# Kernel optimization log

Hardware: AMD Instinct MI355X
Metric: run time of the kernel (lower is better)

Reference implementation:

```python
import jax, jax.numpy as jnp
import numpy as np

T = 4096      # total tokens (flattened batch)
H = 4096      # input_size / hidden dim
O = 4096      # output_size_per_partition
R = 16        # max_lora_rank
L = 8         # max_loras
S = 8         # num_lora_seqs


def setup_inputs() -> dict:
    key = jax.random.key(0)
    k_x, k_w, k_b, k_a, k_bb, k_idx = jax.random.split(key, 6)
    x = jax.random.normal(k_x, (T, H), dtype=jnp.float32)
    weight = jax.random.normal(k_w, (O, H), dtype=jnp.float32) * 0.02
    bias = jax.random.normal(k_b, (O,), dtype=jnp.float32)
    lora_a = jax.random.normal(k_a, (L, H, R), dtype=jnp.float32) * 0.02
    lora_b = jax.random.normal(k_bb, (L, R, O), dtype=jnp.float32) * 0.02
    # indices[i] = (start_idx[i], lora_idx[i]); indices[-1,0] = T (end sentinel).
    # Segment i covers tokens [start[i], start[i+1]) and uses adapter lora_idx[i].
    starts = jnp.arange(S + 1, dtype=jnp.int64) * (T // S)  # monotonically increasing, covers [0, T]
    lora_ids = jax.random.randint(k_idx, (S + 1,), 0, L).astype(jnp.int64)
    indices = jnp.stack([starts, lora_ids], axis=1)  # [S+1, 2]
    return {"x": x, "weight": weight, "bias": bias,
            "lora_a": lora_a, "lora_b": lora_b, "indices": indices}


def reference(x, weight, bias, lora_a, lora_b, indices):
    # Base ColumnParallelLinear: y = x @ W^T + b
    out = jnp.dot(x, weight.T) + bias  # [T, O]

    # Map each token to the LoRA adapter of its segment (SGMV semantics).
    starts = indices[:-1, 0]      # [S]
    seg_lora = indices[:-1, 1]    # [S]
    tok = jnp.arange(x.shape[0])
    seg_of_tok = jnp.searchsorted(starts, tok, side="right") - 1  # [T]
    tok_lora = seg_lora[seg_of_tok]                               # [T]

    # Grouped low-rank GEMM: out[t] += x[t] @ A[lora(t)] @ B[lora(t)].
    # Loop over the small fixed adapter set; mask selects each adapter's tokens.
    n_loras = lora_a.shape[0]
    for l in range(n_loras):
        mask = (tok_lora == l).astype(x.dtype)[:, None]  # [T, 1]
        u = jnp.dot(x * mask, lora_a[l])                 # [T, R] (zero rows off-adapter)
        out = out + jnp.dot(u, lora_b[l])                # [T, O]
    return out
```

## Files before the change

### kernel.cpp

```cpp
#include <hip/hip_runtime.h>
#include <hip/hip_bf16.h>
#include <stdint.h>

#define T_DIM 4096
#define H_DIM 4096
#define O_DIM 4096
#define R_DIM 16
#define S_SEG 8

typedef __attribute__((ext_vector_type(8))) short bf16x8_t;
typedef __attribute__((ext_vector_type(4))) float f32x4_t;

struct ushort4_t { unsigned short x, y, z, w; };

__device__ __forceinline__ unsigned short f2bf(float f) {
  union { float f; unsigned int u; } v; v.f = f;
  unsigned int u = v.u;
  unsigned int r = (u + 0x7fffu + ((u >> 16) & 1u)) >> 16;
  return (unsigned short)r;
}

__device__ __forceinline__ void gload16(const void* g, void* l) {
  __builtin_amdgcn_global_load_lds(
      (const __attribute__((address_space(1))) unsigned int*)g,
      (__attribute__((address_space(3))) unsigned int*)l,
      16, 0, 0);
}

__device__ __forceinline__ int lora_of(const int* __restrict__ indices, int t) {
  int seg = 0;
#pragma unroll
  for (int s = 1; s < S_SEG; ++s)
    if (indices[2 * s] <= t) seg = s;
  return indices[2 * seg + 1];
}

__global__ __launch_bounds__(256) void cvt_kernel(const float* __restrict__ in,
                                                  unsigned short* __restrict__ out,
                                                  int n) {
  int i = (blockIdx.x * 256 + threadIdx.x) * 8;
  if (i >= n) return;
  float4 a = *(const float4*)(in + i);
  float4 b = *(const float4*)(in + i + 4);
  union { unsigned short s[8]; bf16x8_t v; } r;
  r.s[0] = f2bf(a.x); r.s[1] = f2bf(a.y); r.s[2] = f2bf(a.z); r.s[3] = f2bf(a.w);
  r.s[4] = f2bf(b.x); r.s[5] = f2bf(b.y); r.s[6] = f2bf(b.z); r.s[7] = f2bf(b.w);
  *(bf16x8_t*)(out + i) = r.v;
}

__global__ __launch_bounds__(256) void fused_x_kernel(const float* __restrict__ x,
                                                      const float* __restrict__ lora_a,
                                                      const int* __restrict__ indices,
                                                      unsigned short* __restrict__ Xb,
                                                      float* __restrict__ u) {
  const int t0 = blockIdx.x * 4;
  const int tid = threadIdx.x;
  const int l = lora_of(indices, t0);
  const float* __restrict__ a = lora_a + (size_t)l * H_DIM * R_DIM;

  float acc[4][16];
#pragma unroll
  for (int t = 0; t < 4; ++t)
#pragma unroll
    for (int r = 0; r < 16; ++r) acc[t][r] = 0.f;

  for (int h0 = 0; h0 < H_DIM; h0 += 1024) {
    const int h = h0 + tid * 4;
    union { float4 v; float f[4]; } xv[4];
#pragma unroll
    for (int t = 0; t < 4; ++t)
      xv[t].v = *(const float4*)(x + (size_t)(t0 + t) * H_DIM + h);
#pragma unroll
    for (int t = 0; t < 4; ++t) {
      ushort4_t o;
      o.x = f2bf(xv[t].f[0]); o.y = f2bf(xv[t].f[1]);
      o.z = f2bf(xv[t].f[2]); o.w = f2bf(xv[t].f[3]);
      *(ushort4_t*)(Xb + (size_t)(t0 + t) * H_DIM + h) = o;
    }
#pragma unroll
    for (int hh = 0; hh < 4; ++hh) {
      const float4* ap = (const float4*)(a + (size_t)(h + hh) * R_DIM);
      float4 a0 = ap[0], a1 = ap[1], a2 = ap[2], a3 = ap[3];
#pragma unroll
      for (int t = 0; t < 4; ++t) {
        float xs = xv[t].f[hh];
        acc[t][0]  += xs * a0.x; acc[t][1]  += xs * a0.y; acc[t][2]  += xs * a0.z; acc[t][3]  += xs * a0.w;
        acc[t][4]  += xs * a1.x; acc[t][5]  += xs * a1.y; acc[t][6]  += xs * a1.z; acc[t][7]  += xs * a1.w;
        acc[t][8]  += xs * a2.x; acc[t][9]  += xs * a2.y; acc[t][10] += xs * a2.z; acc[t][11] += xs * a2.w;
        acc[t][12] += xs * a3.x; acc[t][13] += xs * a3.y; acc[t][14] += xs * a3.z; acc[t][15] += xs * a3.w;
      }
    }
  }

#pragma unroll
  for (int t = 0; t < 4; ++t)
#pragma unroll
    for (int r = 0; r < 16; ++r)
#pragma unroll
      for (int off = 32; off > 0; off >>= 1)
        acc[t][r] += __shfl_xor(acc[t][r], off, 64);

  __shared__ float red[4][64];
  const int lane = tid & 63, wv = tid >> 6;
  if (lane == 0) {
#pragma unroll
    for (int t = 0; t < 4; ++t)
#pragma unroll
      for (int r = 0; r < 16; ++r) red[wv][t * 16 + r] = acc[t][r];
  }
  __syncthreads();
  if (tid < 64) {
    float s = red[0][tid] + red[1][tid] + red[2][tid] + red[3][tid];
    u[(size_t)t0 * 16 + tid] = s;
  }
}

__global__ __launch_bounds__(256) void gemm_kernel(const unsigned short* __restrict__ A,
                                                   const unsigned short* __restrict__ B,
                                                   const float* __restrict__ bias,
                                                   const float* __restrict__ lora_b,
                                                   const int* __restrict__ indices,
                                                   const float* __restrict__ u,
                                                   float* __restrict__ out) {
  __shared__ unsigned short lds[2 * 128 * 32];
  const int tid = threadIdx.x;
  const int lane = tid & 63;
  const int wid = tid >> 6;
  const int wr = wid >> 1;
  const int wc = wid & 1;
  const int row0 = blockIdx.y * 128;
  const int col0 = blockIdx.x * 128;

  f32x4_t acc[4][4];
#pragma unroll
  for (int m = 0; m < 4; ++m)
#pragma unroll
    for (int n = 0; n < 4; ++n) acc[m][n] = (f32x4_t){0.f, 0.f, 0.f, 0.f};

  const int srow = tid >> 2;
  const int sel = (tid & 3) * 8;
  const unsigned short* aS0 = A + (size_t)(row0 + srow) * H_DIM + sel;
  const unsigned short* aS1 = A + (size_t)(row0 + 64 + srow) * H_DIM + sel;
  const unsigned short* bS0 = B + (size_t)(col0 + srow) * H_DIM + sel;
  const unsigned short* bS1 = B + (size_t)(col0 + 64 + srow) * H_DIM + sel;
  unsigned short* ldsA = lds;
  unsigned short* ldsB = lds + 128 * 32;
  unsigned short* dA0 = ldsA + tid * 8;
  unsigned short* dA1 = ldsA + 2048 + tid * 8;
  unsigned short* dB0 = ldsB + tid * 8;
  unsigned short* dB1 = ldsB + 2048 + tid * 8;

  const unsigned short* aF = ldsA + (size_t)(wr * 64 + (lane & 15)) * 32 + (lane >> 4) * 8;
  const unsigned short* bF = ldsB + (size_t)(wc * 64 + (lane & 15)) * 32 + (lane >> 4) * 8;

  for (int kt = 0; kt < H_DIM; kt += 32) {
    gload16(aS0 + kt, dA0);
    gload16(aS1 + kt, dA1);
    gload16(bS0 + kt, dB0);
    gload16(bS1 + kt, dB1);
    __syncthreads();

    bf16x8_t af[4], bfr[4];
#pragma unroll
    for (int m = 0; m < 4; ++m) af[m] = *(const bf16x8_t*)(aF + m * 16 * 32);
#pragma unroll
    for (int n = 0; n < 4; ++n) bfr[n] = *(const bf16x8_t*)(bF + n * 16 * 32);
#pragma unroll
    for (int m = 0; m < 4; ++m)
#pragma unroll
      for (int n = 0; n < 4; ++n)
        acc[m][n] = __builtin_amdgcn_mfma_f32_16x16x32_bf16(af[m], bfr[n], acc[m][n], 0, 0, 0);
    __syncthreads();
  }

  const int l = lora_of(indices, row0);
  float* uLds = (float*)lds;
  float* bLds = (float*)lds + 2048;
  {
    const float* ug = u + (size_t)row0 * 16;
    int j = tid * 8;
    *(float4*)(uLds + j) = *(const float4*)(ug + j);
    *(float4*)(uLds + j + 4) = *(const float4*)(ug + j + 4);
    int br = tid >> 4, bc = (tid & 15) * 8;
    const float* bg = lora_b + ((size_t)l * R_DIM + br) * O_DIM + col0 + bc;
    *(float4*)(bLds + br * 128 + bc) = *(const float4*)bg;
    *(float4*)(bLds + br * 128 + bc + 4) = *(const float4*)(bg + 4);
  }
  __syncthreads();

  const int rl0 = wr * 64 + (lane >> 4) * 4;
  const int cl0 = wc * 64 + (lane & 15);
#pragma unroll
  for (int r = 0; r < 16; ++r) {
    float b0 = bLds[r * 128 + cl0];
    float b1 = bLds[r * 128 + cl0 + 16];
    float b2 = bLds[r * 128 + cl0 + 32];
    float b3 = bLds[r * 128 + cl0 + 48];
#pragma unroll
    for (int m = 0; m < 4; ++m)
#pragma unroll
      for (int q = 0; q < 4; ++q) {
        float uv = uLds[(rl0 + m * 16 + q) * 16 + r];
        acc[m][0][q] += uv * b0;
        acc[m][1][q] += uv * b1;
        acc[m][2][q] += uv * b2;
        acc[m][3][q] += uv * b3;
      }
  }

  const int r0 = row0 + rl0;
  const int c0 = col0 + cl0;
  float bv[4];
#pragma unroll
  for (int n = 0; n < 4; ++n) bv[n] = bias[c0 + n * 16];
#pragma unroll
  for (int m = 0; m < 4; ++m)
#pragma unroll
    for (int n = 0; n < 4; ++n)
#pragma unroll
      for (int q = 0; q < 4; ++q) {
        int row = r0 + m * 16 + q;
        out[(size_t)row * O_DIM + (c0 + n * 16)] = acc[m][n][q] + bv[n];
      }
}

extern "C" void kernel_launch(void* const* d_in, const int* in_sizes, int n_in,
                              void* d_out, int out_size, void* d_ws, size_t ws_size,
                              hipStream_t stream) {
  const float* x      = (const float*)d_in[0];
  const float* weight = (const float*)d_in[1];
  const float* bias   = (const float*)d_in[2];
  const float* lora_a = (const float*)d_in[3];
  const float* lora_b = (const float*)d_in[4];
  const int*   indices = (const int*)d_in[5];
  float* out = (float*)d_out;

  unsigned short* Xb = (unsigned short*)d_ws;
  unsigned short* Wb = Xb + (size_t)T_DIM * H_DIM;
  float* u = (float*)(Wb + (size_t)O_DIM * H_DIM);

  const int nX = T_DIM * H_DIM;
  cvt_kernel<<<nX / 8 / 256, 256, 0, stream>>>(weight, Wb, nX);
  fused_x_kernel<<<T_DIM / 4, 256, 0, stream>>>(x, lora_a, indices, Xb, u);
  gemm_kernel<<<dim3(O_DIM / 128, T_DIM / 128), 256, 0, stream>>>(Xb, Wb, bias, lora_b, indices, u, out);
}
```

Before: 373.0 us.

## Rewrite GEMM as 256x256 double-buffered tile and transpose LoRA A

New measurement: 361.7 us. 1.03x faster.

```diff
diff --git a/kernel.cpp b/kernel.cpp
--- a/kernel.cpp
+++ b/kernel.cpp
@@ -34,6 +34,10 @@
     if (indices[2 * s] <= t) seg = s;
   return indices[2 * seg + 1];
 }
+
+#define SBAR() do { asm volatile("" ::: "memory"); __builtin_amdgcn_s_barrier(); asm volatile("" ::: "memory"); } while (0)
+#define VMCNT8() asm volatile("s_waitcnt vmcnt(8)" ::: "memory")
+#define VMCNT0() asm volatile("s_waitcnt vmcnt(0)" ::: "memory")
 
 __global__ __launch_bounds__(256) void cvt_kernel(const float* __restrict__ in,
                                                   unsigned short* __restrict__ out,
@@ -48,15 +52,27 @@
   *(bf16x8_t*)(out + i) = r.v;
 }
 
+__global__ __launch_bounds__(256) void transpose_a(const float* __restrict__ a,
+                                                   float* __restrict__ aT) {
+  int l = blockIdx.y;
+  const float* al = a + (size_t)l * H_DIM * R_DIM;
+  float* aTl = aT + (size_t)l * H_DIM * R_DIM;
+  int base = blockIdx.x * 4096;
+  for (int idx = base + threadIdx.x; idx < base + 4096; idx += 256) {
+    int h = idx >> 4, r = idx & 15;
+    aTl[r * H_DIM + h] = al[idx];
+  }
+}
+
 __global__ __launch_bounds__(256) void fused_x_kernel(const float* __restrict__ x,
-                                                      const float* __restrict__ lora_a,
+                                                      const float* __restrict__ aT,
                                                       const int* __restrict__ indices,
                                                       unsigned short* __restrict__ Xb,
                                                       float* __restrict__ u) {
   const int t0 = blockIdx.x * 4;
   const int tid = threadIdx.x;
   const int l = lora_of(indices, t0);
-  const float* __restrict__ a = lora_a + (size_t)l * H_DIM * R_DIM;
+  const float* __restrict__ aTl = aT + (size_t)l * H_DIM * R_DIM;
 
   float acc[4][16];
 #pragma unroll
@@ -64,8 +80,9 @@
 #pragma unroll
     for (int r = 0; r < 16; ++r) acc[t][r] = 0.f;
 
-  for (int h0 = 0; h0 < H_DIM; h0 += 1024) {
-    const int h = h0 + tid * 4;
+#pragma unroll
+  for (int c = 0; c < 4; ++c) {
+    const int h = c * 1024 + tid * 4;
     union { float4 v; float f[4]; } xv[4];
 #pragma unroll
     for (int t = 0; t < 4; ++t)
@@ -78,17 +95,12 @@
       *(ushort4_t*)(Xb + (size_t)(t0 + t) * H_DIM + h) = o;
     }
 #pragma unroll
-    for (int hh = 0; hh < 4; ++hh) {
-      const float4* ap = (const float4*)(a + (size_t)(h + hh) * R_DIM);
-      float4 a0 = ap[0], a1 = ap[1], a2 = ap[2], a3 = ap[3];
-#pragma unroll
-      for (int t = 0; t < 4; ++t) {
-        float xs = xv[t].f[hh];
-        acc[t][0]  += xs * a0.x; acc[t][1]  += xs * a0.y; acc[t][2]  += xs * a0.z; acc[t][3]  += xs * a0.w;
-        acc[t][4]  += xs * a1.x; acc[t][5]  += xs * a1.y; acc[t][6]  += xs * a1.z; acc[t][7]  += xs * a1.w;
-        acc[t][8]  += xs * a2.x; acc[t][9]  += xs * a2.y; acc[t][10] += xs * a2.z; acc[t][11] += xs * a2.w;
-        acc[t][12] += xs * a3.x; acc[t][13] += xs * a3.y; acc[t][14] += xs * a3.z; acc[t][15] += xs * a3.w;
-      }
+    for (int r = 0; r < 16; ++r) {
+      float4 av = *(const float4*)(aTl + (size_t)r * H_DIM + h);
+#pragma unroll
+      for (int t = 0; t < 4; ++t)
+        acc[t][r] += xv[t].f[0] * av.x + xv[t].f[1] * av.y +
+                     xv[t].f[2] * av.z + xv[t].f[3] * av.w;
     }
   }
 
@@ -115,92 +127,210 @@
   }
 }
 
-__global__ __launch_bounds__(256) void gemm_kernel(const unsigned short* __restrict__ A,
-                                                   const unsigned short* __restrict__ B,
-                                                   const float* __restrict__ bias,
-                                                   const float* __restrict__ lora_b,
-                                                   const int* __restrict__ indices,
-                                                   const float* __restrict__ u,
-                                                   float* __restrict__ out) {
-  __shared__ unsigned short lds[2 * 128 * 32];
+__global__ __launch_bounds__(512) void gemm256(const unsigned short* __restrict__ A,
+                                               const unsigned short* __restrict__ B,
+                                               const float* __restrict__ bias,
+                                               const float* __restrict__ lora_b,
+                                               const int* __restrict__ indices,
+                                               const float* __restrict__ u,
+                                               float* __restrict__ out) {
+  extern __shared__ unsigned short lds[];
   const int tid = threadIdx.x;
   const int lane = tid & 63;
   const int wid = tid >> 6;
-  const int wr = wid >> 1;
-  const int wc = wid & 1;
-  const int row0 = blockIdx.y * 128;
-  const int col0 = blockIdx.x * 128;
-
-  f32x4_t acc[4][4];
-#pragma unroll
-  for (int m = 0; m < 4; ++m)
+  const int wr = wid >> 2;
+  const int wc = wid & 3;
+  const int row0 = blockIdx.y * 256;
+  const int col0 = blockIdx.x * 256;
+
+  f32x4_t acc[8][4];
+#pragma unroll
+  for (int m = 0; m < 8; ++m)
 #pragma unroll
     for (int n = 0; n < 4; ++n) acc[m][n] = (f32x4_t){0.f, 0.f, 0.f, 0.f};
 
-  const int srow = tid >> 2;
-  const int sel = (tid & 3) * 8;
-  const unsigned short* aS0 = A + (size_t)(row0 + srow) * H_DIM + sel;
-  const unsigned short* aS1 = A + (size_t)(row0 + 64 + srow) * H_DIM + sel;
-  const unsigned short* bS0 = B + (size_t)(col0 + srow) * H_DIM + sel;
-  const unsigned short* bS1 = B + (size_t)(col0 + 64 + srow) * H_DIM + sel;
-  unsigned short* ldsA = lds;
-  unsigned short* ldsB = lds + 128 * 32;
-  unsigned short* dA0 = ldsA + tid * 8;
-  unsigned short* dA1 = ldsA + 2048 + tid * 8;
-  unsigned short* dB0 = ldsB + tid * 8;
-  unsigned short* dB1 = ldsB + 2048 + tid * 8;
-
-  const unsigned short* aF = ldsA + (size_t)(wr * 64 + (lane & 15)) * 32 + (lane >> 4) * 8;
-  const unsigned short* bF = ldsB + (size_t)(wc * 64 + (lane & 15)) * 32 + (lane >> 4) * 8;
-
-  for (int kt = 0; kt < H_DIM; kt += 32) {
-    gload16(aS0 + kt, dA0);
-    gload16(aS1 + kt, dA1);
-    gload16(bS0 + kt, dB0);
-    gload16(bS1 + kt, dB1);
-    __syncthreads();
-
-    bf16x8_t af[4], bfr[4];
-#pragma unroll
-    for (int m = 0; m < 4; ++m) af[m] = *(const bf16x8_t*)(aF + m * 16 * 32);
-#pragma unroll
-    for (int n = 0; n < 4; ++n) bfr[n] = *(const bf16x8_t*)(bF + n * 16 * 32);
-#pragma unroll
-    for (int m = 0; m < 4; ++m)
-#pragma unroll
-      for (int n = 0; n < 4; ++n)
-        acc[m][n] = __builtin_amdgcn_mfma_f32_16x16x32_bf16(af[m], bfr[n], acc[m][n], 0, 0, 0);
-    __syncthreads();
-  }
+  const int srow = tid >> 3;
+  const int kbyte = ((tid & 7) * 16) ^ (((tid >> 5) & 1) << 5);
+  const unsigned short* aS0 = A + (size_t)(row0 + 0 * 64 + srow) * H_DIM + (kbyte >> 1);
+  const unsigned short* aS1 = A + (size_t)(row0 + 1 * 64 + srow) * H_DIM + (kbyte >> 1);
+  const unsigned short* aS2 = A + (size_t)(row0 + 2 * 64 + srow) * H_DIM + (kbyte >> 1);
+  const unsigned short* aS3 = A + (size_t)(row0 + 3 * 64 + srow) * H_DIM + (kbyte >> 1);
+  const unsigned short* bS0 = B + (size_t)(col0 + 0 * 64 + srow) * H_DIM + (kbyte >> 1);
+  const unsigned short* bS1 = B + (size_t)(col0 + 1 * 64 + srow) * H_DIM + (kbyte >> 1);
+  const unsigned short* bS2 = B + (size_t)(col0 + 2 * 64 + srow) * H_DIM + (kbyte >> 1);
+  const unsigned short* bS3 = B + (size_t)(col0 + 3 * 64 + srow) * H_DIM + (kbyte >> 1);
+
+#define STAGE(kt, d) do {                                                  \
+    unsigned short* La_ = lds + (d) * 16384;                               \
+    unsigned short* Lb_ = lds + 32768 + (d) * 16384;                       \
+    gload16(aS0 + (kt), La_ + tid * 8);                                    \
+    gload16(aS1 + (kt), La_ + 4096 + tid * 8);                             \
+    gload16(aS2 + (kt), La_ + 8192 + tid * 8);                             \
+    gload16(aS3 + (kt), La_ + 12288 + tid * 8);                            \
+    gload16(bS0 + (kt), Lb_ + tid * 8);                                    \
+    gload16(bS1 + (kt), Lb_ + 4096 + tid * 8);                             \
+    gload16(bS2 + (kt), Lb_ + 8192 + tid * 8);                             \
+    gload16(bS3 + (kt), Lb_ + 12288 + tid * 8);                            \
+  } while (0)
+
+  const int rA = wr * 128 + (lane & 15);
+  const int rB = wc * 64 + (lane & 15);
+  const int aBase = rA * 64;
+  const int bBase = rB * 64;
+  const int ks0 = ((((lane >> 4) * 16)) ^ ((lane & 4) << 3)) >> 1;
+  const int ks1 = (((64 + (lane >> 4) * 16)) ^ ((lane & 4) << 3)) >> 1;
+
+  STAGE(0, 0);
+  STAGE(64, 1);
+  VMCNT8();
+  SBAR();
+
+#pragma unroll 2
+  for (int t = 0; t < H_DIM / 64; ++t) {
+    const int cur = t & 1;
+    const unsigned short* La = lds + cur * 16384;
+    const unsigned short* Lb = lds + 32768 + cur * 16384;
+
+    bf16x8_t b0, b1, b2, b3, a0, a1, a2, a3;
+    b0 = *(const bf16x8_t*)(Lb + bBase + 0 * 1024 + ks0);
+    b1 = *(const bf16x8_t*)(Lb + bBase + 1 * 1024 + ks0);
+    b2 = *(const bf16x8_t*)(Lb + bBase + 2 * 1024 + ks0);
+    b3 = *(const bf16x8_t*)(Lb + bBase + 3 * 1024 + ks0);
+    a0 = *(const bf16x8_t*)(La + aBase + 0 * 1024 + ks0);
+    a1 = *(const bf16x8_t*)(La + aBase + 1 * 1024 + ks0);
+    a2 = *(const bf16x8_t*)(La + aBase + 2 * 1024 + ks0);
+    a3 = *(const bf16x8_t*)(La + aBase + 3 * 1024 + ks0);
+    __builtin_amdgcn_s_setprio(1);
+    acc[0][0] = __builtin_amdgcn_mfma_f32_16x16x32_bf16(a0, b0, acc[0][0], 0, 0, 0);
+    acc[0][1] = __builtin_amdgcn_mfma_f32_16x16x32_bf16(a0, b1, acc[0][1], 0, 0, 0);
+    acc[0][2] = __builtin_amdgcn_mfma_f32_16x16x32_bf16(a0, b2, acc[0][2], 0, 0, 0);
+    acc[0][3] = __builtin_amdgcn_mfma_f32_16x16x32_bf16(a0, b3, acc[0][3], 0, 0, 0);
+    acc[1][0] = __builtin_amdgcn_mfma_f32_16x16x32_bf16(a1, b0, acc[1][0], 0, 0, 0);
+    acc[1][1] = __builtin_amdgcn_mfma_f32_16x16x32_bf16(a1, b1, acc[1][1], 0, 0, 0);
+    acc[1][2] = __builtin_amdgcn_mfma_f32_16x16x32_bf16(a1, b2, acc[1][2], 0, 0, 0);
+    acc[1][3] = __builtin_amdgcn_mfma_f32_16x16x32_bf16(a1, b3, acc[1][3], 0, 0, 0);
+    acc[2][0] = __builtin_amdgcn_mfma_f32_16x16x32_bf16(a2, b0, acc[2][0], 0, 0, 0);
+    acc[2][1] = __builtin_amdgcn_mfma_f32_16x16x32_bf16(a2, b1, acc[2][1], 0, 0, 0);
+    acc[2][2] = __builtin_amdgcn_mfma_f32_16x16x32_bf16(a2, b2, acc[2][2], 0, 0, 0);
+    acc[2][3] = __builtin_amdgcn_mfma_f32_16x16x32_bf16(a2, b3, acc[2][3], 0, 0, 0);
+    acc[3][0] = __builtin_amdgcn_mfma_f32_16x16x32_bf16(a3, b0, acc[3][0], 0, 0, 0);
+    acc[3][1] = __builtin_amdgcn_mfma_f32_16x16x32_bf16(a3, b1, acc[3][1], 0, 0, 0);
+    acc[3][2] = __builtin_amdgcn_mfma_f32_16x16x32_bf16(a3, b2, acc[3][2], 0, 0, 0);
+    acc[3][3] = __builtin_amdgcn_mfma_f32_16x16x32_bf16(a3, b3, acc[3][3], 0, 0, 0);
+    __builtin_amdgcn_s_setprio(0);
+
+    bf16x8_t c0, c1, c2, c3;
+    c0 = *(const bf16x8_t*)(Lb + bBase + 0 * 1024 + ks1);
+    c1 = *(const bf16x8_t*)(Lb + bBase + 1 * 1024 + ks1);
+    c2 = *(const bf16x8_t*)(Lb + bBase + 2 * 1024 + ks1);
+    c3 = *(const bf16x8_t*)(Lb + bBase + 3 * 1024 + ks1);
+    a0 = *(const bf16x8_t*)(La + aBase + 0 * 1024 + ks1);
+    a1 = *(const bf16x8_t*)(La + aBase + 1 * 1024 + ks1);
+    a2 = *(const bf16x8_t*)(La + aBase + 2 * 1024 + ks1);
+    a3 = *(const bf16x8_t*)(La + aBase + 3 * 1024 + ks1);
+    __builtin_amdgcn_s_setprio(1);
+    acc[0][0] = __builtin_amdgcn_mfma_f32_16x16x32_bf16(a0, c0, acc[0][0], 0, 0, 0);
+    acc[0][1] = __builtin_amdgcn_mfma_f32_16x16x32_bf16(a0, c1, acc[0][1], 0, 0, 0);
+    acc[0][2] = __builtin_amdgcn_mfma_f32_16x16x32_bf16(a0, c2, acc[0][2], 0, 0, 0);
+    acc[0][3] = __builtin_amdgcn_mfma_f32_16x16x32_bf16(a0, c3, acc[0][3], 0, 0, 0);
+    acc[1][0] = __builtin_amdgcn_mfma_f32_16x16x32_bf16(a1, c0, acc[1][0], 0, 0, 0);
+    acc[1][1] = __builtin_amdgcn_mfma_f32_16x16x32_bf16(a1, c1, acc[1][1], 0, 0, 0);
+    acc[1][2] = __builtin_amdgcn_mfma_f32_16x16x32_bf16(a1, c2, acc[1][2], 0, 0, 0);
+    acc[1][3] = __builtin_amdgcn_mfma_f32_16x16x32_bf16(a1, c3, acc[1][3], 0, 0, 0);
+    acc[2][0] = __builtin_amdgcn_mfma_f32_16x16x32_bf16(a2, c0, acc[2][0], 0, 0, 0);
+    acc[2][1] = __builtin_amdgcn_mfma_f32_16x16x32_bf16(a2, c1, acc[2][1], 0, 0, 0);
+    acc[2][2] = __builtin_amdgcn_mfma_f32_16x16x32_bf16(a2, c2, acc[2][2], 0, 0, 0);
+    acc[2][3] = __builtin_amdgcn_mfma_f32_16x16x32_bf16(a2, c3, acc[2][3], 0, 0, 0);
+    acc[3][0] = __builtin_amdgcn_mfma_f32_16x16x32_bf16(a3, c0, acc[3][0], 0, 0, 0);
+    acc[3][1] = __builtin_amdgcn_mfma_f32_16x16x32_bf16(a3, c1, acc[3][1], 0, 0, 0);
+    acc[3][2] = __builtin_amdgcn_mfma_f32_16x16x32_bf16(a3, c2, acc[3][2], 0, 0, 0);
+    acc[3][3] = __builtin_amdgcn_mfma_f32_16x16x32_bf16(a3, c3, acc[3][3], 0, 0, 0);
+    __builtin_amdgcn_s_setprio(0);
+
+    a0 = *(const bf16x8_t*)(La + aBase + 4 * 1024 + ks0);
+    a1 = *(const bf16x8_t*)(La + aBase + 5 * 1024 + ks0);
+    a2 = *(const bf16x8_t*)(La + aBase + 6 * 1024 + ks0);
+    a3 = *(const bf16x8_t*)(La + aBase + 7 * 1024 + ks0);
+    __builtin_amdgcn_s_setprio(1);
+    acc[4][0] = __builtin_amdgcn_mfma_f32_16x16x32_bf16(a0, b0, acc[4][0], 0, 0, 0);
+    acc[4][1] = __builtin_amdgcn_mfma_f32_16x16x32_bf16(a0, b1, acc[4][1], 0, 0, 0);
+    acc[4][2] = __builtin_amdgcn_mfma_f32_16x16x32_bf16(a0, b2, acc[4][2], 0, 0, 0);
+    acc[4][3] = __builtin_amdgcn_mfma_f32_16x16x32_bf16(a0, b3, acc[4][3], 0, 0, 0);
+    acc[5][0] = __builtin_amdgcn_mfma_f32_16x16x32_bf16(a1, b0, acc[5][0], 0, 0, 0);
+    acc[5][1] = __builtin_amdgcn_mfma_f32_16x16x32_bf16(a1, b1, acc[5][1], 0, 0, 0);
+    acc[5][2] = __builtin_amdgcn_mfma_f32_16x16x32_bf16(a1, b2, acc[5][2], 0, 0, 0);
+    acc[5][3] = __builtin_amdgcn_mfma_f32_16x16x32_bf16(a1, b3, acc[5][3], 0, 0, 0);
+    acc[6][0] = __builtin_amdgcn_mfma_f32_16x16x32_bf16(a2, b0, acc[6][0], 0, 0, 0);
+    acc[6][1] = __builtin_amdgcn_mfma_f32_16x16x32_bf16(a2, b1, acc[6][1], 0, 0, 0);
+    acc[6][2] = __builtin_amdgcn_mfma_f32_16x16x32_bf16(a2, b2, acc[6][2], 0, 0, 0);
+    acc[6][3] = __builtin_amdgcn_mfma_f32_16x16x32_bf16(a2, b3, acc[6][3], 0, 0, 0);
+    acc[7][0] = __builtin_amdgcn_mfma_f32_16x16x32_bf16(a3, b0, acc[7][0], 0, 0, 0);
+    acc[7][1] = __builtin_amdgcn_mfma_f32_16x16x32_bf16(a3, b1, acc[7][1], 0, 0, 0);
+    acc[7][2] = __builtin_amdgcn_mfma_f32_16x16x32_bf16(a3, b2, acc[7][2], 0, 0, 0);
+    acc[7][3] = __builtin_amdgcn_mfma_f32_16x16x32_bf16(a3, b3, acc[7][3], 0, 0, 0);
+    __builtin_amdgcn_s_setprio(0);
+
+    a0 = *(const bf16x8_t*)(La + aBase + 4 * 1024 + ks1);
+    a1 = *(const bf16x8_t*)(La + aBase + 5 * 1024 + ks1);
+    a2 = *(const bf16x8_t*)(La + aBase + 6 * 1024 + ks1);
+    a3 = *(const bf16x8_t*)(La + aBase + 7 * 1024 + ks1);
+    __builtin_amdgcn_s_setprio(1);
+    acc[4][0] = __builtin_amdgcn_mfma_f32_16x16x32_bf16(a0, c0, acc[4][0], 0, 0, 0);
+    acc[4][1] = __builtin_amdgcn_mfma_f32_16x16x32_bf16(a0, c1, acc[4][1], 0, 0, 0);
+    acc[4][2] = __builtin_amdgcn_mfma_f32_16x16x32_bf16(a0, c2, acc[4][2], 0, 0, 0);
+    acc[4][3] = __builtin_amdgcn_mfma_f32_16x16x32_bf16(a0, c3, acc[4][3], 0, 0, 0);
+    acc[5][0] = __builtin_amdgcn_mfma_f32_16x16x32_bf16(a1, c0, acc[5][0], 0, 0, 0);
+    acc[5][1] = __builtin_amdgcn_mfma_f32_16x16x32_bf16(a1, c1, acc[5][1], 0, 0, 0);
+    acc[5][2] = __builtin_amdgcn_mfma_f32_16x16x32_bf16(a1, c2, acc[5][2], 0, 0, 0);
+    acc[5][3] = __builtin_amdgcn_mfma_f32_16x16x32_bf16(a1, c3, acc[5][3], 0, 0, 0);
+    acc[6][0] = __builtin_amdgcn_mfma_f32_16x16x32_bf16(a2, c0, acc[6][0], 0, 0, 0);
+    acc[6][1] = __builtin_amdgcn_mfma_f32_16x16x32_bf16(a2, c1, acc[6][1], 0, 0, 0);
+    acc[6][2] = __builtin_amdgcn_mfma_f32_16x16x32_bf16(a2, c2, acc[6][2], 0, 0, 0);
+    acc[6][3] = __builtin_amdgcn_mfma_f32_16x16x32_bf16(a2, c3, acc[6][3], 0, 0, 0);
+    acc[7][0] = __builtin_amdgcn_mfma_f32_16x16x32_bf16(a3, c0, acc[7][0], 0, 0, 0);
+    acc[7][1] = __builtin_amdgcn_mfma_f32_16x16x32_bf16(a3, c1, acc[7][1], 0, 0, 0);
+    acc[7][2] = __builtin_amdgcn_mfma_f32_16x16x32_bf16(a3, c2, acc[7][2], 0, 0, 0);
+    acc[7][3] = __builtin_amdgcn_mfma_f32_16x16x32_bf16(a3, c3, acc[7][3], 0, 0, 0);
+    __builtin_amdgcn_s_setprio(0);
+
+    SBAR();
+    if (t + 2 < H_DIM / 64) {
+      STAGE((t + 2) * 64, cur);
+      VMCNT8();
+    } else {
+      VMCNT0();
+    }
+    SBAR();
+  }
+#undef STAGE
 
   const int l = lora_of(indices, row0);
-  float* uLds = (float*)lds;
-  float* bLds = (float*)lds + 2048;
+  float* uL = (float*)lds;
+  float* bL = (float*)lds + 4096;
   {
     const float* ug = u + (size_t)row0 * 16;
-    int j = tid * 8;
-    *(float4*)(uLds + j) = *(const float4*)(ug + j);
-    *(float4*)(uLds + j + 4) = *(const float4*)(ug + j + 4);
-    int br = tid >> 4, bc = (tid & 15) * 8;
+    *(float4*)(uL + tid * 8) = *(const float4*)(ug + tid * 8);
+    *(float4*)(uL + tid * 8 + 4) = *(const float4*)(ug + tid * 8 + 4);
+    int br = tid >> 5, bc = (tid & 31) * 8;
     const float* bg = lora_b + ((size_t)l * R_DIM + br) * O_DIM + col0 + bc;
-    *(float4*)(bLds + br * 128 + bc) = *(const float4*)bg;
-    *(float4*)(bLds + br * 128 + bc + 4) = *(const float4*)(bg + 4);
-  }
-  __syncthreads();
-
-  const int rl0 = wr * 64 + (lane >> 4) * 4;
+    *(float4*)(bL + br * 256 + bc) = *(const float4*)bg;
+    *(float4*)(bL + br * 256 + bc + 4) = *(const float4*)(bg + 4);
+  }
+  SBAR();
+
   const int cl0 = wc * 64 + (lane & 15);
+  const int rl0 = wr * 128 + (lane >> 4) * 4;
 #pragma unroll
   for (int r = 0; r < 16; ++r) {
-    float b0 = bLds[r * 128 + cl0];
-    float b1 = bLds[r * 128 + cl0 + 16];
-    float b2 = bLds[r * 128 + cl0 + 32];
-    float b3 = bLds[r * 128 + cl0 + 48];
-#pragma unroll
-    for (int m = 0; m < 4; ++m)
+    float b0 = bL[r * 256 + cl0];
+    float b1 = bL[r * 256 + cl0 + 16];
+    float b2 = bL[r * 256 + cl0 + 32];
+    float b3 = bL[r * 256 + cl0 + 48];
+#pragma unroll
+    for (int m = 0; m < 8; ++m)
 #pragma unroll
       for (int q = 0; q < 4; ++q) {
-        float uv = uLds[(rl0 + m * 16 + q) * 16 + r];
+        float uv = uL[(rl0 + m * 16 + q) * 16 + r];
         acc[m][0][q] += uv * b0;
         acc[m][1][q] += uv * b1;
         acc[m][2][q] += uv * b2;
@@ -208,19 +338,17 @@
       }
   }
 
-  const int r0 = row0 + rl0;
-  const int c0 = col0 + cl0;
   float bv[4];
 #pragma unroll
-  for (int n = 0; n < 4; ++n) bv[n] = bias[c0 + n * 16];
-#pragma unroll
-  for (int m = 0; m < 4; ++m)
+  for (int n = 0; n < 4; ++n) bv[n] = bias[col0 + cl0 + n * 16];
+#pragma unroll
+  for (int m = 0; m < 8; ++m)
 #pragma unroll
     for (int n = 0; n < 4; ++n)
 #pragma unroll
       for (int q = 0; q < 4; ++q) {
-        int row = r0 + m * 16 + q;
-        out[(size_t)row * O_DIM + (c0 + n * 16)] = acc[m][n][q] + bv[n];
+        int row = row0 + rl0 + m * 16 + q;
+        out[(size_t)row * O_DIM + (col0 + cl0 + n * 16)] = acc[m][n][q] + bv[n];
       }
 }
 
@@ -238,9 +366,15 @@
   unsigned short* Xb = (unsigned short*)d_ws;
   unsigned short* Wb = Xb + (size_t)T_DIM * H_DIM;
   float* u = (float*)(Wb + (size_t)O_DIM * H_DIM);
+  float* aT = (float*)Wb;
+
+  hipFuncSetAttribute((const void*)gemm256,
+                      hipFuncAttributeMaxDynamicSharedMemorySize, 131072);
 
   const int nX = T_DIM * H_DIM;
+  transpose_a<<<dim3(16, 8), 256, 0, stream>>>(lora_a, aT);
+  fused_x_kernel<<<T_DIM / 4, 256, 0, stream>>>(x, aT, indices, Xb, u);
   cvt_kernel<<<nX / 8 / 256, 256, 0, stream>>>(weight, Wb, nX);
-  fused_x_kernel<<<T_DIM / 4, 256, 0, stream>>>(x, lora_a, indices, Xb, u);
-  gemm_kernel<<<dim3(O_DIM / 128, T_DIM / 128), 256, 0, stream>>>(Xb, Wb, bias, lora_b, indices, u, out);
-}
+  gemm256<<<dim3(O_DIM / 256, T_DIM / 256), 512, 131072, stream>>>(
+      Xb, Wb, bias, lora_b, indices, u, out);
+}
```
